# Performance work log

Hardware: AMD Instinct MI355X
Metric: run time of the kernel (lower is better)

The kernel has to match this reference:

```python
import jax, jax.numpy as jnp
import numpy as np

EPS = 1e-5  # BatchNorm eps (torch default)
PAD = 1
K = 9  # 3x3 kernel points

def conv3x3(x, w, b):
    # x: [B,C,H,W], w: [O,C,3,3]
    y = jax.lax.conv_general_dilated(x, w, (1, 1), ((PAD, PAD), (PAD, PAD)),
                                     dimension_numbers=('NCHW', 'OIHW', 'NCHW'))
    return y + b[None, :, None, None]

def deform_conv2d(x, offset, mask, weight, bias):
    # Modulated deformable conv v2, stride 1, pad 1, 3x3 kernel.
    # x: [B,C,H,W]; offset: [B,2K,H,W] (first K = dy, last K = dx); mask: [B,K,H,W]
    B, C, H, W = x.shape
    ki, kj = jnp.meshgrid(jnp.arange(3), jnp.arange(3), indexing='ij')
    ki = ki.reshape(K).astype(x.dtype)
    kj = kj.reshape(K).astype(x.dtype)
    dy = offset[:, :K].transpose(0, 2, 3, 1)   # [B,H,W,K]
    dx = offset[:, K:].transpose(0, 2, 3, 1)
    m = mask.transpose(0, 2, 3, 1)             # [B,H,W,K]
    hs = jnp.arange(H, dtype=x.dtype)
    ws = jnp.arange(W, dtype=x.dtype)
    py = hs[None, :, None, None] - PAD + ki[None, None, None, :] + dy  # [B,H,W,K]
    px = ws[None, None, :, None] - PAD + kj[None, None, None, :] + dx
    y0 = jnp.floor(py)
    x0 = jnp.floor(px)
    wy1 = py - y0
    wx1 = px - x0
    wy0 = 1.0 - wy1
    wx0 = 1.0 - wx1

    def gather(yi, xi):
        valid = ((yi >= 0) & (yi < H) & (xi >= 0) & (xi < W)).astype(x.dtype)
        yc = jnp.clip(yi, 0, H - 1).astype(jnp.int32)
        xc = jnp.clip(xi, 0, W - 1).astype(jnp.int32)
        g = jax.vmap(lambda img, yb, xb: img[:, yb, xb])(x, yc, xc)  # [B,C,H,W,K]
        return g * valid[:, None]

    val = (gather(y0, x0) * (wy0 * wx0)[:, None]
           + gather(y0, x0 + 1.0) * (wy0 * wx1)[:, None]
           + gather(y0 + 1.0, x0) * (wy1 * wx0)[:, None]
           + gather(y0 + 1.0, x0 + 1.0) * (wy1 * wx1)[:, None])
    val = val * m[:, None]  # modulation
    out = jnp.einsum('bchwk,ock->bohw', val, weight.reshape(weight.shape[0], C, K))
    return out + bias[None, :, None, None]

def dcnv2(x, w_om, b_om, w, b, gamma, beta, mean, var):
    om = conv3x3(x, w_om, b_om)               # [B,27,H,W]
    o1, o2, mr = jnp.split(om, 3, axis=1)
    offset = jnp.concatenate([o1, o2], axis=1)  # [B,18,H,W]
    mask = jax.nn.sigmoid(mr)
    y = deform_conv2d(x, offset, mask, w, b)
    scale = (gamma / jnp.sqrt(var + EPS))[None, :, None, None]
    y = (y - mean[None, :, None, None]) * scale + beta[None, :, None, None]
    return jax.nn.silu(y)

def setup_inputs() -> dict:
    key = jax.random.key(0)
    ks = jax.random.split(key, 9)
    B, C, H, W = 4, 256, 128, 128
    C4 = C // 4
    return {
        'x': jax.random.normal(ks[0], (B, C, H, W), jnp.float32),
        'w': jax.random.normal(ks[1], (4, C4, C4, 3, 3), jnp.float32) * 0.05,
        'b': jax.random.normal(ks[2], (4, C4), jnp.float32) * 0.05,
        'w_om': jax.random.normal(ks[3], (4, 27, C4, 3, 3), jnp.float32) * 0.01,
        'b_om': jax.random.normal(ks[4], (4, 27), jnp.float32) * 0.01,
        'gamma': jax.random.normal(ks[5], (4, C4), jnp.float32) * 0.1 + 1.0,
        'beta': jax.random.normal(ks[6], (4, C4), jnp.float32) * 0.1,
        'mean': jax.random.normal(ks[7], (4, C4), jnp.float32) * 0.1,
        'var': jax.random.uniform(ks[8], (4, C4), jnp.float32, minval=0.5, maxval=1.5),
    }

def reference(x, w, b, w_om, b_om, gamma, beta, mean, var):
    B, C, H, W = x.shape
    C4 = C // 4
    # channel-split into 4 independent groups, vmap identical DCNv2 over groups
    xg = x.reshape(B, 4, C4, H, W).transpose(1, 0, 2, 3, 4)  # [4,B,C4,H,W]
    yg = jax.vmap(dcnv2)(xg, w_om, b_om, w, b, gamma, beta, mean, var)
    return yg.transpose(1, 0, 2, 3, 4).reshape(B, C, H, W)
```

## Files before the change

kernel.cpp:

```cpp
#include <hip/hip_runtime.h>
#include <math.h>

#define Hs 128
#define Ws 128
#define HWs 16384

typedef __attribute__((ext_vector_type(8))) short short8;
typedef __attribute__((ext_vector_type(8))) __bf16 bf16x8;
typedef __attribute__((ext_vector_type(4))) float f32x4;

static __device__ __forceinline__ float bf2f(unsigned short u) {
    union { unsigned int i; float f; } v; v.i = ((unsigned int)u) << 16; return v.f;
}
static __device__ __forceinline__ unsigned short f2bf(float f) {
    unsigned int u = __builtin_bit_cast(unsigned int, f);
    return (unsigned short)((u + 0x7fffu + ((u >> 16) & 1u)) >> 16);
}
static __device__ __forceinline__ unsigned int pack2bf(float a0, float a1) {
    return (unsigned int)f2bf(a0) | ((unsigned int)f2bf(a1) << 16);
}
static __device__ __forceinline__ f32x4 mfma16(short8 a, short8 b, f32x4 c) {
    return __builtin_amdgcn_mfma_f32_16x16x32_bf16(
        __builtin_bit_cast(bf16x8, a), __builtin_bit_cast(bf16x8, b), c, 0, 0, 0);
}

__global__ __launch_bounds__(256) void k_xt(const float* __restrict__ x,
                                            const float* __restrict__ w,
                                            const float* __restrict__ b,
                                            const float* __restrict__ w_om,
                                            const float* __restrict__ gamma,
                                            const float* __restrict__ beta,
                                            const float* __restrict__ mean,
                                            const float* __restrict__ var,
                                            unsigned short* __restrict__ xT,
                                            unsigned short* __restrict__ w2,
                                            unsigned short* __restrict__ wom2,
                                            float* __restrict__ scsh) {
    const int tid = threadIdx.x;
    const int flatb = blockIdx.y * 256 + blockIdx.x;
    if (flatb < 576) {
        int idx = flatb * 256 + tid;
        if (idx < 4 * 64 * 576) {
            int go = idx / 576;
            int ck = idx - go * 576;
            int k = ck >> 6, c = ck & 63;
            w2[idx] = f2bf(w[go * 576 + c * 9 + k]);
        }
        if (idx < 4 * 32 * 576) {
            int gj = idx / 576;
            int g = gj >> 5, j = gj & 31;
            int ck = idx - gj * 576;
            int k = ck >> 6, c = ck & 63;
            float v = (j < 27) ? w_om[(g * 27 + j) * 576 + c * 9 + k] : 0.f;
            wom2[idx] = f2bf(v);
        }
        if (idx < 256) {
            float sc = gamma[idx] * rsqrtf(var[idx] + 1e-5f);
            scsh[idx] = sc;
            scsh[256 + idx] = (b[idx] - mean[idx]) * sc + beta[idx];
        }
    }

    const int img = blockIdx.y;
    const int g = img >> 2, bb = img & 3;
    const int p0 = blockIdx.x * 64;
    __shared__ float t[64 * 65];

    const float* xg = x + (size_t)(bb * 256 + g * 64) * HWs + p0;
    const int pr = tid & 63, cw = tid >> 6;
#pragma unroll
    for (int i = 0; i < 16; ++i) {
        int c = i * 4 + cw;
        t[c * 65 + pr] = xg[(size_t)c * HWs + pr];
    }
    __syncthreads();
    const int p = tid >> 2, c16 = (tid & 3) * 16;
    unsigned short* dst = xT + (size_t)img * HWs * 64 + (size_t)(p0 + p) * 64 + c16;
    unsigned int rr[8];
#pragma unroll
    for (int q = 0; q < 8; ++q)
        rr[q] = pack2bf(t[(c16 + 2 * q) * 65 + p], t[(c16 + 2 * q + 1) * 65 + p]);
    *(uint4*)dst       = make_uint4(rr[0], rr[1], rr[2], rr[3]);
    *(uint4*)(dst + 8) = make_uint4(rr[4], rr[5], rr[6], rr[7]);
}

__global__ __launch_bounds__(256, 2) void k_off(const unsigned short* __restrict__ xT,
                                                const unsigned short* __restrict__ wom2,
                                                const float* __restrict__ b_om,
                                                float* __restrict__ om) {
    const int img = blockIdx.y;
    const int g = img >> 2;
    const int h = blockIdx.x;
    const int tid = threadIdx.x;
    const int lane = tid & 63, wv = tid >> 6;
    const int mt = wv & 1, nh = wv >> 1;
    const int m = lane & 15, q = lane >> 4;

    __shared__ unsigned short xrow[3 * 130 * 72];

    const unsigned short* xTi = xT + (size_t)img * HWs * 64;
    for (int i = tid; i < 3 * 130 * 8; i += 256) {
        int rr = i / 1040;
        int rem = i - rr * 1040;
        int px = rem >> 3, j = rem & 7;
        int gh = h + rr - 1, gw = px - 1;
        uint4 v = make_uint4(0, 0, 0, 0);
        if (gh >= 0 && gh < Hs && gw >= 0 && gw < Ws)
            v = *(const uint4*)(xTi + (size_t)(gh * Ws + gw) * 64 + j * 8);
        *(uint4*)&xrow[(rr * 130 + px) * 72 + j * 8] = v;
    }

    short8 afrag[18];
    const unsigned short* wb = wom2 + (size_t)(g * 32 + mt * 16 + m) * 576 + q * 8;
#pragma unroll
    for (int t = 0; t < 18; ++t) afrag[t] = *(const short8*)(wb + t * 32);

    f32x4 acc[4];
#pragma unroll
    for (int t = 0; t < 4; ++t) acc[t] = (f32x4){0.f, 0.f, 0.f, 0.f};

    __syncthreads();

#pragma unroll
    for (int k = 0; k < 9; ++k) {
        const int ki = k / 3, kj = k - ki * 3;
#pragma unroll
        for (int s = 0; s < 2; ++s) {
#pragma unroll
            for (int t = 0; t < 4; ++t) {
                int px = (nh * 4 + t) * 16 + m + kj;
                short8 bfrag = *(const short8*)&xrow[(ki * 130 + px) * 72 + (s * 4 + q) * 8];
                acc[t] = mfma16(afrag[k * 2 + s], bfrag, acc[t]);
            }
        }
    }

    float* omi = om + (size_t)img * 27 * HWs + h * Ws;
#pragma unroll
    for (int t = 0; t < 4; ++t) {
#pragma unroll
        for (int r = 0; r < 4; ++r) {
            int j = mt * 16 + q * 4 + r;
            if (j < 27) {
                float v = acc[t][r] + b_om[g * 27 + j];
                if (j >= 18) v = 1.f / (1.f + __expf(-v));
                omi[(size_t)j * HWs + (nh * 4 + t) * 16 + m] = v;
            }
        }
    }
}

__global__ __launch_bounds__(256, 3) void k_def(const unsigned short* __restrict__ xT,
                                                const float* __restrict__ om,
                                                const unsigned short* __restrict__ w2,
                                                const float* __restrict__ scsh,
                                                float* __restrict__ out) {
    const int img = blockIdx.y;
    const int g = img >> 2, bb = img & 3;
    const int p0 = blockIdx.x * 64;
    const int tid = threadIdx.x;
    const int lane = tid & 63, wv = tid >> 6;
    const int m = lane & 15, q = lane >> 4;

    __shared__ int   pO[4][576];
    __shared__ float pW[4][576];
    __shared__ unsigned short val[2][64 * 72];
    __shared__ float lsc[64], lsh[64];

    if (tid < 64) {
        lsc[tid] = scsh[g * 64 + tid];
        lsh[tid] = scsh[256 + g * 64 + tid];
    }

    const float* omg = om + (size_t)img * 27 * HWs;
    for (int idx = tid; idx < 576; idx += 256) {
        int k = idx >> 6, pp = idx & 63;
        int p = p0 + pp;
        int h = p >> 7, w = p & 127;
        float dy = omg[k * HWs + p];
        float dx = omg[(9 + k) * HWs + p];
        float mk = omg[(18 + k) * HWs + p];
        int ki = k / 3, kj = k - ki * 3;
        float py = (float)(h - 1 + ki) + dy;
        float px = (float)(w - 1 + kj) + dx;
        float fy = floorf(py), fx = floorf(px);
        float wy1 = py - fy, wx1 = px - fx;
        float wy0 = 1.f - wy1, wx0 = 1.f - wx1;
        int y0 = (int)fy, x0 = (int)fx, y1 = y0 + 1, x1 = x0 + 1;
        bool vy0 = (y0 >= 0) && (y0 < Hs), vy1 = (y1 >= 0) && (y1 < Hs);
        bool vx0 = (x0 >= 0) && (x0 < Ws), vx1 = (x1 >= 0) && (x1 < Ws);
        int cy0 = min(max(y0, 0), Hs - 1), cy1 = min(max(y1, 0), Hs - 1);
        int cx0 = min(max(x0, 0), Ws - 1), cx1 = min(max(x1, 0), Ws - 1);
        pO[0][idx] = cy0 * Ws + cx0;
        pO[1][idx] = cy0 * Ws + cx1;
        pO[2][idx] = cy1 * Ws + cx0;
        pO[3][idx] = cy1 * Ws + cx1;
        pW[0][idx] = (vy0 && vx0) ? wy0 * wx0 * mk : 0.f;
        pW[1][idx] = (vy0 && vx1) ? wy0 * wx1 * mk : 0.f;
        pW[2][idx] = (vy1 && vx0) ? wy1 * wx0 * mk : 0.f;
        pW[3][idx] = (vy1 && vx1) ? wy1 * wx1 * mk : 0.f;
    }

    short8 afrag[18];
    const unsigned short* wb = w2 + (size_t)(g * 64 + wv * 16 + m) * 576 + q * 8;
#pragma unroll
    for (int t = 0; t < 18; ++t) afrag[t] = *(const short8*)(wb + t * 32);

    f32x4 acc[4];
#pragma unroll
    for (int t = 0; t < 4; ++t) acc[t] = (f32x4){0.f, 0.f, 0.f, 0.f};

    const unsigned short* xTi = xT + (size_t)img * HWs * 64;
    const int p = tid >> 2, c4 = tid & 3;

    __syncthreads();

    uint4 gth[8];
    float wf0, wf1, wf2, wf3;
    auto fetch = [&](int k) {
        const int kb = k * 64 + p;
        const int off0 = pO[0][kb], off1 = pO[1][kb], off2 = pO[2][kb], off3 = pO[3][kb];
        wf0 = pW[0][kb]; wf1 = pW[1][kb]; wf2 = pW[2][kb]; wf3 = pW[3][kb];
        const unsigned short* s0 = xTi + (size_t)off0 * 64;
        const unsigned short* s1 = xTi + (size_t)off1 * 64;
        const unsigned short* s2 = xTi + (size_t)off2 * 64;
        const unsigned short* s3 = xTi + (size_t)off3 * 64;
        gth[0] = *(const uint4*)(s0 + c4 * 8);
        gth[1] = *(const uint4*)(s1 + c4 * 8);
        gth[2] = *(const uint4*)(s2 + c4 * 8);
        gth[3] = *(const uint4*)(s3 + c4 * 8);
        gth[4] = *(const uint4*)(s0 + (c4 + 4) * 8);
        gth[5] = *(const uint4*)(s1 + (c4 + 4) * 8);
        gth[6] = *(const uint4*)(s2 + (c4 + 4) * 8);
        gth[7] = *(const uint4*)(s3 + (c4 + 4) * 8);
    };
    fetch(0);

#pragma unroll
    for (int k = 0; k < 9; ++k) {
        unsigned short* vb = &val[k & 1][0];
#pragma unroll
        for (int it = 0; it < 2; ++it) {
            const int oc8 = (c4 + it * 4) * 8;
            unsigned int rr[4];
#pragma unroll
            for (int e = 0; e < 4; ++e) {
                const unsigned int u0 = ((const unsigned int*)&gth[it * 4 + 0])[e];
                const unsigned int u1 = ((const unsigned int*)&gth[it * 4 + 1])[e];
                const unsigned int u2 = ((const unsigned int*)&gth[it * 4 + 2])[e];
                const unsigned int u3 = ((const unsigned int*)&gth[it * 4 + 3])[e];
                float a0 = wf0 * bf2f((unsigned short)(u0 & 0xffff))
                         + wf1 * bf2f((unsigned short)(u1 & 0xffff))
                         + wf2 * bf2f((unsigned short)(u2 & 0xffff))
                         + wf3 * bf2f((unsigned short)(u3 & 0xffff));
                float a1 = wf0 * bf2f((unsigned short)(u0 >> 16))
                         + wf1 * bf2f((unsigned short)(u1 >> 16))
                         + wf2 * bf2f((unsigned short)(u2 >> 16))
                         + wf3 * bf2f((unsigned short)(u3 >> 16));
                rr[e] = pack2bf(a0, a1);
            }
            *(uint4*)&vb[p * 72 + oc8] = make_uint4(rr[0], rr[1], rr[2], rr[3]);
        }
        if (k < 8) fetch(k + 1);
        __syncthreads();
        const unsigned short* vr = &val[k & 1][0];
#pragma unroll
        for (int s = 0; s < 2; ++s) {
#pragma unroll
            for (int t = 0; t < 4; ++t) {
                short8 bfrag = *(const short8*)&vr[(t * 16 + m) * 72 + s * 32 + q * 8];
                acc[t] = mfma16(afrag[k * 2 + s], bfrag, acc[t]);
            }
        }
    }

    float* outg = out + ((size_t)bb * 256 + g * 64) * HWs + p0;
#pragma unroll
    for (int t = 0; t < 4; ++t) {
#pragma unroll
        for (int r = 0; r < 4; ++r) {
            int o = wv * 16 + q * 4 + r;
            float y = acc[t][r] * lsc[o] + lsh[o];
            outg[(size_t)o * HWs + t * 16 + m] = y / (1.f + __expf(-y));
        }
    }
}

extern "C" void kernel_launch(void* const* d_in, const int* in_sizes, int n_in,
                              void* d_out, int out_size, void* d_ws, size_t ws_size,
                              hipStream_t stream) {
    const float* x     = (const float*)d_in[0];
    const float* w     = (const float*)d_in[1];
    const float* b     = (const float*)d_in[2];
    const float* w_om  = (const float*)d_in[3];
    const float* b_om  = (const float*)d_in[4];
    const float* gamma = (const float*)d_in[5];
    const float* beta  = (const float*)d_in[6];
    const float* mean  = (const float*)d_in[7];
    const float* var   = (const float*)d_in[8];
    float* out = (float*)d_out;

    char* ws = (char*)d_ws;
    float* om            = (float*)ws;
    unsigned short* xT   = (unsigned short*)(ws + 28311552);
    unsigned short* w2   = (unsigned short*)(ws + 61865984);
    unsigned short* wom2 = (unsigned short*)(ws + 62160896);
    float* scsh          = (float*)(ws + 62308352);

    hipLaunchKernelGGL(k_xt, dim3(256, 16), dim3(256), 0, stream,
                       x, w, b, w_om, gamma, beta, mean, var, xT, w2, wom2, scsh);
    hipLaunchKernelGGL(k_off, dim3(128, 16), dim3(256), 0, stream, xT, wom2, b_om, om);
    hipLaunchKernelGGL(k_def, dim3(256, 16), dim3(256), 0, stream, xT, om, w2, scsh, out);
}
```

Before: 273.4 us.

## Double-buffer gather registers, use packed FP32 math, swizzle LDS tile

The gather for kernel point k+1 is now issued before the blend of point k, using two register buffers so loads overlap the bilinear arithmetic. The blend uses v_pk_mul/v_pk_fma on channel pairs and a hardware bf16 pack conversion in place of scalar math and software rounding. The LDS value tile drops its 72-element row padding in favour of an XOR swizzle, and each thread now gathers 16 contiguous channels. The extra gather buffer raises register pressure, which may hurt occupancy at the 3-blocks launch bound.

Result: faster. 261.1 us (-4.5%).

```diff
diff --git a/kernel.cpp b/kernel.cpp
--- a/kernel.cpp
+++ b/kernel.cpp
@@ -8,6 +8,7 @@
 typedef __attribute__((ext_vector_type(8))) short short8;
 typedef __attribute__((ext_vector_type(8))) __bf16 bf16x8;
 typedef __attribute__((ext_vector_type(4))) float f32x4;
+typedef __attribute__((ext_vector_type(2))) float f32x2;
 
 static __device__ __forceinline__ float bf2f(unsigned short u) {
     union { unsigned int i; float f; } v; v.i = ((unsigned int)u) << 16; return v.f;
@@ -22,6 +23,27 @@
 static __device__ __forceinline__ f32x4 mfma16(short8 a, short8 b, f32x4 c) {
     return __builtin_amdgcn_mfma_f32_16x16x32_bf16(
         __builtin_bit_cast(bf16x8, a), __builtin_bit_cast(bf16x8, b), c, 0, 0, 0);
+}
+static __device__ __forceinline__ f32x2 pk_mul(f32x2 a, f32x2 b) {
+    f32x2 d;
+    asm("v_pk_mul_f32 %0, %1, %2" : "=v"(d) : "v"(a), "v"(b));
+    return d;
+}
+static __device__ __forceinline__ f32x2 pk_fma(f32x2 a, f32x2 b, f32x2 c) {
+    f32x2 d;
+    asm("v_pk_fma_f32 %0, %1, %2, %3" : "=v"(d) : "v"(a), "v"(b), "v"(c));
+    return d;
+}
+static __device__ __forceinline__ unsigned int cvt_pk_bf16(float lo, float hi) {
+    unsigned int d;
+    asm("v_cvt_pk_bf16_f32 %0, %1, %2" : "=v"(d) : "v"(lo), "v"(hi));
+    return d;
+}
+static __device__ __forceinline__ f32x2 bfpair(unsigned int u) {
+    union { unsigned int i[2]; f32x2 f; } v;
+    v.i[0] = u << 16;
+    v.i[1] = u & 0xffff0000u;
+    return v.f;
 }
 
 __global__ __launch_bounds__(256) void k_xt(const float* __restrict__ x,
@@ -164,7 +186,7 @@
 
     __shared__ int   pO[4][576];
     __shared__ float pW[4][576];
-    __shared__ unsigned short val[2][64 * 72];
+    __shared__ unsigned short val[2][64 * 64];
     __shared__ float lsc[64], lsh[64];
 
     if (tid < 64) {
@@ -212,63 +234,67 @@
 
     const unsigned short* xTi = xT + (size_t)img * HWs * 64;
     const int p = tid >> 2, c4 = tid & 3;
+    const int wr_sw = ((p >> 1) & 7) << 3;
+    const int rd_sw = ((m >> 1) & 7) << 3;
 
     __syncthreads();
 
-    uint4 gth[8];
-    float wf0, wf1, wf2, wf3;
-    auto fetch = [&](int k) {
+    uint4 gth[2][8];
+    float wfb[2][4];
+    auto fetch = [&](int k, int bf) {
         const int kb = k * 64 + p;
         const int off0 = pO[0][kb], off1 = pO[1][kb], off2 = pO[2][kb], off3 = pO[3][kb];
-        wf0 = pW[0][kb]; wf1 = pW[1][kb]; wf2 = pW[2][kb]; wf3 = pW[3][kb];
-        const unsigned short* s0 = xTi + (size_t)off0 * 64;
-        const unsigned short* s1 = xTi + (size_t)off1 * 64;
-        const unsigned short* s2 = xTi + (size_t)off2 * 64;
-        const unsigned short* s3 = xTi + (size_t)off3 * 64;
-        gth[0] = *(const uint4*)(s0 + c4 * 8);
-        gth[1] = *(const uint4*)(s1 + c4 * 8);
-        gth[2] = *(const uint4*)(s2 + c4 * 8);
-        gth[3] = *(const uint4*)(s3 + c4 * 8);
-        gth[4] = *(const uint4*)(s0 + (c4 + 4) * 8);
-        gth[5] = *(const uint4*)(s1 + (c4 + 4) * 8);
-        gth[6] = *(const uint4*)(s2 + (c4 + 4) * 8);
-        gth[7] = *(const uint4*)(s3 + (c4 + 4) * 8);
+        wfb[bf][0] = pW[0][kb]; wfb[bf][1] = pW[1][kb];
+        wfb[bf][2] = pW[2][kb]; wfb[bf][3] = pW[3][kb];
+        const unsigned short* s0 = xTi + (size_t)off0 * 64 + c4 * 16;
+        const unsigned short* s1 = xTi + (size_t)off1 * 64 + c4 * 16;
+        const unsigned short* s2 = xTi + (size_t)off2 * 64 + c4 * 16;
+        const unsigned short* s3 = xTi + (size_t)off3 * 64 + c4 * 16;
+        gth[bf][0] = *(const uint4*)(s0);
+        gth[bf][1] = *(const uint4*)(s1);
+        gth[bf][2] = *(const uint4*)(s2);
+        gth[bf][3] = *(const uint4*)(s3);
+        gth[bf][4] = *(const uint4*)(s0 + 8);
+        gth[bf][5] = *(const uint4*)(s1 + 8);
+        gth[bf][6] = *(const uint4*)(s2 + 8);
+        gth[bf][7] = *(const uint4*)(s3 + 8);
     };
-    fetch(0);
+    fetch(0, 0);
 
 #pragma unroll
     for (int k = 0; k < 9; ++k) {
-        unsigned short* vb = &val[k & 1][0];
+        const int cb = k & 1, nb = cb ^ 1;
+        if (k < 8) fetch(k + 1, nb);
+        unsigned short* vb = &val[cb][0];
+        const float* wf = wfb[cb];
+        f32x2 w0p = {wf[0], wf[0]}, w1p = {wf[1], wf[1]};
+        f32x2 w2p = {wf[2], wf[2]}, w3p = {wf[3], wf[3]};
 #pragma unroll
         for (int it = 0; it < 2; ++it) {
-            const int oc8 = (c4 + it * 4) * 8;
+            const int oc8 = (2 * c4 + it) * 8;
             unsigned int rr[4];
 #pragma unroll
             for (int e = 0; e < 4; ++e) {
-                const unsigned int u0 = ((const unsigned int*)&gth[it * 4 + 0])[e];
-                const unsigned int u1 = ((const unsigned int*)&gth[it * 4 + 1])[e];
-                const unsigned int u2 = ((const unsigned int*)&gth[it * 4 + 2])[e];
-                const unsigned int u3 = ((const unsigned int*)&gth[it * 4 + 3])[e];
-                float a0 = wf0 * bf2f((unsigned short)(u0 & 0xffff))
-                         + wf1 * bf2f((unsigned short)(u1 & 0xffff))
-                         + wf2 * bf2f((unsigned short)(u2 & 0xffff))
-                         + wf3 * bf2f((unsigned short)(u3 & 0xffff));
-                float a1 = wf0 * bf2f((unsigned short)(u0 >> 16))
-                         + wf1 * bf2f((unsigned short)(u1 >> 16))
-                         + wf2 * bf2f((unsigned short)(u2 >> 16))
-                         + wf3 * bf2f((unsigned short)(u3 >> 16));
-                rr[e] = pack2bf(a0, a1);
+                f32x2 x0 = bfpair(((const unsigned int*)&gth[cb][it * 4 + 0])[e]);
+                f32x2 x1 = bfpair(((const unsigned int*)&gth[cb][it * 4 + 1])[e]);
+                f32x2 x2 = bfpair(((const unsigned int*)&gth[cb][it * 4 + 2])[e]);
+                f32x2 x3 = bfpair(((const unsigned int*)&gth[cb][it * 4 + 3])[e]);
+                f32x2 a = pk_mul(x0, w0p);
+                a = pk_fma(x1, w1p, a);
+                a = pk_fma(x2, w2p, a);
+                a = pk_fma(x3, w3p, a);
+                rr[e] = cvt_pk_bf16(a[0], a[1]);
             }
-            *(uint4*)&vb[p * 72 + oc8] = make_uint4(rr[0], rr[1], rr[2], rr[3]);
-        }
-        if (k < 8) fetch(k + 1);
+            *(uint4*)&vb[p * 64 + (oc8 ^ wr_sw)] = make_uint4(rr[0], rr[1], rr[2], rr[3]);
+        }
         __syncthreads();
-        const unsigned short* vr = &val[k & 1][0];
+        const unsigned short* vr = &val[cb][0];
 #pragma unroll
         for (int s = 0; s < 2; ++s) {
 #pragma unroll
             for (int t = 0; t < 4; ++t) {
-                short8 bfrag = *(const short8*)&vr[(t * 16 + m) * 72 + s * 32 + q * 8];
+                const int row = t * 16 + m;
+                short8 bfrag = *(const short8*)&vr[row * 64 + ((s * 32 + q * 8) ^ rd_sw)];
                 acc[t] = mfma16(afrag[k * 2 + s], bfrag, acc[t]);
             }
         }
```
